# Kernel tuning notes

Measured on AMD Instinct MI355X. Metric: run time of the kernel, lower is better.

Reference implementation:

```python
import jax, jax.numpy as jnp
import numpy as np

# dims: B=batch, N1=in_channels (primary caps), P=pcap_n_dims, N2=n_caps, D=n_dims
B, N1, P, N2, D = 64, 1152, 8, 128, 16
ROUTINGS = 2


def squash(s, axis=-1):
    # squash_factor * unit_vector, with eps-stabilized norm (matches torch.finfo eps)
    sq_norm = jnp.sum(s * s, axis=axis, keepdims=True)
    norm = jnp.sqrt(sq_norm + jnp.finfo(s.dtype).eps)
    return (sq_norm / (1.0 + sq_norm)) * (s / norm)


def setup_inputs() -> dict:
    key = jax.random.key(0)
    k1, k2 = jax.random.split(key)
    x = jax.random.normal(k1, (B, N1, P), dtype=jnp.float32)
    # learned transform W: nn.Parameter(torch.randn(1, N1, N2, D, P)); leading 1 dropped
    W = jax.random.normal(k2, (N1, N2, D, P), dtype=jnp.float32)
    return {"x": x, "W": W}


def reference(x, W):
    b, n1 = x.shape[0], x.shape[1]
    n2 = W.shape[1]
    # caps2_predicted[b,i,n,d] = sum_p W[i,n,d,p] * x[b,i,p]  (the tiled batched matmul)
    pred = jnp.einsum('indp,bip->bind', W, x)  # [B, N1, N2, D]
    raw = jnp.zeros((b, n1, n2), dtype=pred.dtype)  # routing logits
    v = None
    for i in range(ROUTINGS):
        c = jax.nn.softmax(raw, axis=2)                  # softmax over output capsules
        s = jnp.einsum('bin,bind->bnd', c, pred)         # weighted sum over input caps
        v = squash(s, axis=-1)                           # [B, N2, D]
        if i < ROUTINGS - 1:
            # agreement: <prediction, output> over the D dimension
            raw = raw + jnp.einsum('bind,bnd->bin', pred, v)
    return v  # [B, n_caps, n_dims]
```

## Files before the change

kernel.cpp:

```cpp
#include <hip/hip_runtime.h>
#include <math.h>

#define B_   64
#define P_   8
#define N1_  1152
#define N2_  128
#define D_   16

#define NSPLIT 16
#define CHUNK  (N1_ / NSPLIT)
#define NIB    (CHUNK / 4)

typedef __attribute__((ext_vector_type(8)))  short bf16x8;
typedef __attribute__((ext_vector_type(4)))  float f32x4;
typedef __attribute__((ext_vector_type(16))) float f32x16;

__device__ inline void split_frag(float4 a0, float4 a1, bf16x8& hi, bf16x8& lo)
{
    float w[8] = {a0.x, a0.y, a0.z, a0.w, a1.x, a1.y, a1.z, a1.w};
#pragma unroll
    for (int j = 0; j < 8; ++j) {
        unsigned ub = __float_as_uint(w[j]);
        hi[j] = (short)(ub >> 16);
        float hif = __uint_as_float(ub & 0xffff0000u);
        float r = w[j] - hif;
        lo[j] = (short)(__float_as_uint(r) >> 16);
    }
}

__device__ inline void split_arr(const float* w, bf16x8& hi, bf16x8& lo)
{
#pragma unroll
    for (int j = 0; j < 8; ++j) {
        unsigned ub = __float_as_uint(w[j]);
        hi[j] = (short)(ub >> 16);
        float hif = __uint_as_float(ub & 0xffff0000u);
        float r = w[j] - hif;
        lo[j] = (short)(__float_as_uint(r) >> 16);
    }
}

__device__ inline void split4_pack(float4 s, uint2& hp, uint2& lp)
{
    float w[4] = {s.x, s.y, s.z, s.w};
    unsigned hs[4], ls[4];
#pragma unroll
    for (int j = 0; j < 4; ++j) {
        unsigned ub = __float_as_uint(w[j]);
        hs[j] = ub >> 16;
        float hif = __uint_as_float(ub & 0xffff0000u);
        float r = w[j] - hif;
        ls[j] = __float_as_uint(r) >> 16;
    }
    hp.x = hs[0] | (hs[1] << 16); hp.y = hs[2] | (hs[3] << 16);
    lp.x = ls[0] | (ls[1] << 16); lp.y = ls[2] | (ls[3] << 16);
}

__device__ inline unsigned short bf16_rne(float x, float& deq)
{
    unsigned ub = __float_as_uint(x);
    unsigned r  = ub + 0x7fffu + ((ub >> 16) & 1u);
    unsigned short us = (unsigned short)(r >> 16);
    deq = __uint_as_float(((unsigned)us) << 16);
    return us;
}

__global__ __launch_bounds__(128) void k0_xt(const float* __restrict__ x,
                                             float* __restrict__ xt,
                                             unsigned short* __restrict__ xth,
                                             unsigned short* __restrict__ xtl,
                                             float* __restrict__ denom)
{
    const int i  = blockIdx.x;
    const int t  = threadIdx.x;
    const int b  = t >> 1, ph = t & 1;
    float4 v = *(const float4*)(x + ((size_t)b * N1_ + i) * P_ + ph * 4);
    const size_t off = (size_t)i * (64 * P_) + b * P_ + ph * 4;
    *(float4*)(xt + off) = v;
    uint2 hp, lp;
    split4_pack(v, hp, lp);
    *(uint2*)(xth + off) = hp;
    *(uint2*)(xtl + off) = lp;
    int z = i * 128 + t;
    if (z < N1_ * 64) denom[z] = 0.f;
}

__global__ __launch_bounds__(256) void k1_s0_mfma(const unsigned short* __restrict__ xth,
                                                  const unsigned short* __restrict__ xtl,
                                                  const float* __restrict__ W,
                                                  float* __restrict__ s0p)
{
    const int tid   = threadIdx.x;
    const int lane  = tid & 63;
    const int wv    = tid >> 6;
    const int col   = lane & 15;
    const int quad  = lane >> 4;
    const int n     = blockIdx.x * 4 + wv;
    const int isp   = blockIdx.y;
    const int ibase = isp * CHUNK;

    f32x4 acc[4];
#pragma unroll
    for (int bt = 0; bt < 4; ++bt) acc[bt] = (f32x4){0.f, 0.f, 0.f, 0.f};

    for (int ib = 0; ib < NIB; ++ib) {
        const int iq = ibase + ib * 4 + quad;
        const float* wp = W + ((size_t)iq * N2_ + n) * (D_ * P_) + col * P_;
        float4 wa = *(const float4*)wp;
        float4 wb = *(const float4*)(wp + 4);
        bf16x8 ahi, alo;
        split_frag(wa, wb, ahi, alo);
#pragma unroll
        for (int bt = 0; bt < 4; ++bt) {
            const int b = bt * 16 + col;
            const size_t xo = (size_t)iq * (64 * P_) + b * P_;
            bf16x8 bhi = *(const bf16x8*)(xth + xo);
            bf16x8 blo = *(const bf16x8*)(xtl + xo);
            acc[bt] = __builtin_amdgcn_mfma_f32_16x16x32_bf16(ahi, bhi, acc[bt], 0, 0, 0);
            acc[bt] = __builtin_amdgcn_mfma_f32_16x16x32_bf16(ahi, blo, acc[bt], 0, 0, 0);
            acc[bt] = __builtin_amdgcn_mfma_f32_16x16x32_bf16(alo, bhi, acc[bt], 0, 0, 0);
        }
    }
#pragma unroll
    for (int bt = 0; bt < 4; ++bt) {
        const int b = bt * 16 + col;
        float4 v = make_float4(acc[bt][0], acc[bt][1], acc[bt][2], acc[bt][3]);
        *(float4*)(s0p + (size_t)isp * (B_ * N2_ * D_) + (size_t)b * (N2_ * D_)
                   + n * D_ + quad * 4) = v;
    }
}

__global__ __launch_bounds__(256) void k2_squash(const float* __restrict__ spart,
                                                 float* __restrict__ vout,
                                                 unsigned short* __restrict__ v0h,
                                                 unsigned short* __restrict__ v0l,
                                                 float scale, int nsplit)
{
    int idx = blockIdx.x * 256 + threadIdx.x;
    float4 s = make_float4(0.f, 0.f, 0.f, 0.f);
    for (int sp = 0; sp < nsplit; ++sp) {
        float4 t = *(const float4*)(spart + (size_t)sp * (B_ * N2_ * D_) + (size_t)idx * 4);
        s.x += t.x; s.y += t.y; s.z += t.z; s.w += t.w;
    }
    s.x *= scale; s.y *= scale; s.z *= scale; s.w *= scale;
    float sq = s.x * s.x + s.y * s.y + s.z * s.z + s.w * s.w;
    sq += __shfl_xor(sq, 1);
    sq += __shfl_xor(sq, 2);
    float norm = sqrtf(sq + 1.1920929e-7f);
    float f = (sq / (1.f + sq)) / norm;
    float4 o = make_float4(s.x * f, s.y * f, s.z * f, s.w * f);
    *(float4*)(vout + (size_t)idx * 4) = o;
    if (v0h) {
        uint2 hp, lp;
        split4_pack(o, hp, lp);
        *(uint2*)(v0h + (size_t)idx * 4) = hp;
        *(uint2*)(v0l + (size_t)idx * 4) = lp;
    }
}

__global__ __launch_bounds__(256) void k3a2_mfma32(const float* __restrict__ xt,
                                                   const float* __restrict__ W,
                                                   const unsigned short* __restrict__ v0h,
                                                   const unsigned short* __restrict__ v0l,
                                                   unsigned short* __restrict__ e_t,
                                                   float* __restrict__ denom)
{
    const int tid  = threadIdx.x;
    const int lane = tid & 63;
    const int wv   = tid >> 6;
    const int m    = lane & 31;
    const int kh   = lane >> 5;
    const int isub = m >> 3;
    const int p    = m & 7;
    const int i0   = blockIdx.y * 4;
    const int nbase = blockIdx.x * 32 + wv * 8;

    float4 xq0[4], xq1[4];
#pragma unroll
    for (int is = 0; is < 4; ++is) {
        const float* xp = xt + (size_t)(i0 + is) * (64 * P_) + m * 8 + kh * 4;
        xq0[is] = *(const float4*)xp;
        xq1[is] = *(const float4*)(xp + 256);
    }

    float dacc[4] = {0.f, 0.f, 0.f, 0.f};

#pragma unroll 1
    for (int nt = 0; nt < 8; ++nt) {
        const int n = nbase + nt;

        bf16x8 vhi[2], vlo[2];
#pragma unroll
        for (int bt = 0; bt < 2; ++bt) {
            const size_t vo = (size_t)(bt * 32 + m) * (N2_ * D_) + n * D_ + kh * 8;
            vhi[bt] = *(const bf16x8*)(v0h + vo);
            vlo[bt] = *(const bf16x8*)(v0l + vo);
        }

        const float* wp = W + ((size_t)(i0 + isub) * N2_ + n) * (D_ * P_) + kh * 64 + p;
        float a[8];
#pragma unroll
        for (int j = 0; j < 8; ++j) a[j] = wp[8 * j];
        bf16x8 ahi, alo;
        split_arr(a, ahi, alo);

        f32x16 acc0, acc1;
#pragma unroll
        for (int r = 0; r < 16; ++r) { acc0[r] = 0.f; acc1[r] = 0.f; }
        acc0 = __builtin_amdgcn_mfma_f32_32x32x16_bf16(ahi, vhi[0], acc0, 0, 0, 0);
        acc0 = __builtin_amdgcn_mfma_f32_32x32x16_bf16(ahi, vlo[0], acc0, 0, 0, 0);
        acc0 = __builtin_amdgcn_mfma_f32_32x32x16_bf16(alo, vhi[0], acc0, 0, 0, 0);
        acc1 = __builtin_amdgcn_mfma_f32_32x32x16_bf16(ahi, vhi[1], acc1, 0, 0, 0);
        acc1 = __builtin_amdgcn_mfma_f32_32x32x16_bf16(ahi, vlo[1], acc1, 0, 0, 0);
        acc1 = __builtin_amdgcn_mfma_f32_32x32x16_bf16(alo, vhi[1], acc1, 0, 0, 0);

#pragma unroll
        for (int is = 0; is < 4; ++is) {
            float r0 = acc0[4 * is] * xq0[is].x + acc0[4 * is + 1] * xq0[is].y
                     + acc0[4 * is + 2] * xq0[is].z + acc0[4 * is + 3] * xq0[is].w;
            float r1 = acc1[4 * is] * xq1[is].x + acc1[4 * is + 1] * xq1[is].y
                     + acc1[4 * is + 2] * xq1[is].z + acc1[4 * is + 3] * xq1[is].w;
            r0 += __shfl_xor(r0, 32);
            r1 += __shfl_xor(r1, 32);
            float e = __expf(kh ? r1 : r0);
            float er;
            unsigned short eb = bf16_rne(e, er);
            e_t[(size_t)(i0 + is) * (N2_ * 64) + n * 64 + kh * 32 + m] = eb;
            dacc[is] += er;
        }
    }

    __shared__ float dred[4][4][64];
#pragma unroll
    for (int is = 0; is < 4; ++is) dred[wv][is][kh * 32 + m] = dacc[is];
    __syncthreads();
    {
        const int is = tid >> 6;
        const int b  = tid & 63;
        float s = dred[0][is][b] + dred[1][is][b] + dred[2][is][b] + dred[3][is][b];
        atomicAdd(&denom[(size_t)(i0 + is) * 64 + b], s);
    }
}

__global__ __launch_bounds__(256) void k3c_s1_mfma(const float* __restrict__ xt,
                                                   const float* __restrict__ W,
                                                   const unsigned short* __restrict__ e_t,
                                                   const float* __restrict__ denom,
                                                   float* __restrict__ s1p)
{
    const int tid   = threadIdx.x;
    const int lane  = tid & 63;
    const int wv    = tid >> 6;
    const int col   = lane & 15;
    const int quad  = lane >> 4;
    const int n     = blockIdx.x * 4 + wv;
    const int isp   = blockIdx.y;
    const int ibase = isp * CHUNK;

    f32x4 acc[4];
#pragma unroll
    for (int bt = 0; bt < 4; ++bt) acc[bt] = (f32x4){0.f, 0.f, 0.f, 0.f};

    for (int ib = 0; ib < NIB; ++ib) {
        const int iq = ibase + ib * 4 + quad;
        const float* wp = W + ((size_t)iq * N2_ + n) * (D_ * P_) + col * P_;
        float4 wa = *(const float4*)wp;
        float4 wb = *(const float4*)(wp + 4);
        bf16x8 ahi, alo;
        split_frag(wa, wb, ahi, alo);
#pragma unroll
        for (int bt = 0; bt < 4; ++bt) {
            const int b = bt * 16 + col;
            const float* xp = xt + (size_t)iq * (64 * P_) + b * P_;
            float4 xa = *(const float4*)xp;
            float4 xb = *(const float4*)(xp + 4);
            float e  = __uint_as_float((unsigned)e_t[((size_t)iq * N2_ + n) * 64 + b] << 16);
            float dv = denom[(size_t)iq * 64 + b];
            float c  = e * __builtin_amdgcn_rcpf(dv);
            float4 ya = make_float4(xa.x * c, xa.y * c, xa.z * c, xa.w * c);
            float4 yb = make_float4(xb.x * c, xb.y * c, xb.z * c, xb.w * c);
            bf16x8 bhi, blo;
            split_frag(ya, yb, bhi, blo);
            acc[bt] = __builtin_amdgcn_mfma_f32_16x16x32_bf16(ahi, bhi, acc[bt], 0, 0, 0);
            acc[bt] = __builtin_amdgcn_mfma_f32_16x16x32_bf16(ahi, blo, acc[bt], 0, 0, 0);
            acc[bt] = __builtin_amdgcn_mfma_f32_16x16x32_bf16(alo, bhi, acc[bt], 0, 0, 0);
        }
    }
#pragma unroll
    for (int bt = 0; bt < 4; ++bt) {
        const int b = bt * 16 + col;
        float4 v = make_float4(acc[bt][0], acc[bt][1], acc[bt][2], acc[bt][3]);
        *(float4*)(s1p + (size_t)isp * (B_ * N2_ * D_) + (size_t)b * (N2_ * D_)
                   + n * D_ + quad * 4) = v;
    }
}

extern "C" void kernel_launch(void* const* d_in, const int* in_sizes, int n_in,
                              void* d_out, int out_size, void* d_ws, size_t ws_size,
                              hipStream_t stream)
{
    const float* x = (const float*)d_in[0];
    const float* W = (const float*)d_in[1];
    float* out = (float*)d_out;

    float* s_part = (float*)d_ws;
    float* v0     = s_part + (size_t)NSPLIT * B_ * N2_ * D_;
    float* xt     = v0 + B_ * N2_ * D_;
    float* denom  = xt + (size_t)N1_ * 64 * P_;
    unsigned short* xth = (unsigned short*)(denom + (size_t)N1_ * 64);
    unsigned short* xtl = xth + (size_t)N1_ * 64 * P_;
    unsigned short* v0h = xtl + (size_t)N1_ * 64 * P_;
    unsigned short* v0l = v0h + (size_t)B_ * N2_ * D_;
    unsigned short* e_t = v0l + (size_t)B_ * N2_ * D_;

    k0_xt       <<<N1_,               128, 0, stream>>>(x, xt, xth, xtl, denom);
    k1_s0_mfma  <<<dim3(32, NSPLIT),  256, 0, stream>>>(xth, xtl, W, s_part);
    k2_squash   <<<128,               256, 0, stream>>>(s_part, v0, v0h, v0l, 1.f / 128.f, NSPLIT);
    k3a2_mfma32 <<<dim3(4, N1_ / 4),  256, 0, stream>>>(xt, W, v0h, v0l, e_t, denom);
    k3c_s1_mfma <<<dim3(32, NSPLIT),  256, 0, stream>>>(xt, W, e_t, denom, s_part);
    k2_squash   <<<128,               256, 0, stream>>>(s_part, out, nullptr, nullptr, 1.f, NSPLIT);
}
```

Before: 188.4 us.

## Drop x transpose kernel; read x directly and give k3a2 full-n blocks

Removes the k0 transpose/split kernel and has the MFMA kernels read x in its original layout, splitting it to bf16 hi/lo in registers instead. k3a2 now uses 1024-thread blocks covering all 128 output capsules for a 4-row slab of i. The per-block denominator sum is written directly instead of through atomics, which also removes the need to zero denom beforehand. This saves one launch and the workspace traffic for xt, xth and xtl. In exchange, x reads are strided by N1*P across the batch, and k1 redoes the split arithmetic in each block.

```diff
diff --git a/kernel.cpp b/kernel.cpp
--- a/kernel.cpp
+++ b/kernel.cpp
@@ -65,28 +65,7 @@
     return us;
 }
 
-__global__ __launch_bounds__(128) void k0_xt(const float* __restrict__ x,
-                                             float* __restrict__ xt,
-                                             unsigned short* __restrict__ xth,
-                                             unsigned short* __restrict__ xtl,
-                                             float* __restrict__ denom)
-{
-    const int i  = blockIdx.x;
-    const int t  = threadIdx.x;
-    const int b  = t >> 1, ph = t & 1;
-    float4 v = *(const float4*)(x + ((size_t)b * N1_ + i) * P_ + ph * 4);
-    const size_t off = (size_t)i * (64 * P_) + b * P_ + ph * 4;
-    *(float4*)(xt + off) = v;
-    uint2 hp, lp;
-    split4_pack(v, hp, lp);
-    *(uint2*)(xth + off) = hp;
-    *(uint2*)(xtl + off) = lp;
-    int z = i * 128 + t;
-    if (z < N1_ * 64) denom[z] = 0.f;
-}
-
-__global__ __launch_bounds__(256) void k1_s0_mfma(const unsigned short* __restrict__ xth,
-                                                  const unsigned short* __restrict__ xtl,
+__global__ __launch_bounds__(256) void k1_s0_mfma(const float* __restrict__ x,
                                                   const float* __restrict__ W,
                                                   float* __restrict__ s0p)
 {
@@ -113,9 +92,11 @@
 #pragma unroll
         for (int bt = 0; bt < 4; ++bt) {
             const int b = bt * 16 + col;
-            const size_t xo = (size_t)iq * (64 * P_) + b * P_;
-            bf16x8 bhi = *(const bf16x8*)(xth + xo);
-            bf16x8 blo = *(const bf16x8*)(xtl + xo);
+            const float* xp = x + ((size_t)b * N1_ + iq) * P_;
+            float4 xa = *(const float4*)xp;
+            float4 xb = *(const float4*)(xp + 4);
+            bf16x8 bhi, blo;
+            split_frag(xa, xb, bhi, blo);
             acc[bt] = __builtin_amdgcn_mfma_f32_16x16x32_bf16(ahi, bhi, acc[bt], 0, 0, 0);
             acc[bt] = __builtin_amdgcn_mfma_f32_16x16x32_bf16(ahi, blo, acc[bt], 0, 0, 0);
             acc[bt] = __builtin_amdgcn_mfma_f32_16x16x32_bf16(alo, bhi, acc[bt], 0, 0, 0);
@@ -158,12 +139,12 @@
     }
 }
 
-__global__ __launch_bounds__(256) void k3a2_mfma32(const float* __restrict__ xt,
-                                                   const float* __restrict__ W,
-                                                   const unsigned short* __restrict__ v0h,
-                                                   const unsigned short* __restrict__ v0l,
-                                                   unsigned short* __restrict__ e_t,
-                                                   float* __restrict__ denom)
+__global__ __launch_bounds__(1024) void k3a2_mfma32(const float* __restrict__ x,
+                                                    const float* __restrict__ W,
+                                                    const unsigned short* __restrict__ v0h,
+                                                    const unsigned short* __restrict__ v0l,
+                                                    unsigned short* __restrict__ e_t,
+                                                    float* __restrict__ denom)
 {
     const int tid  = threadIdx.x;
     const int lane = tid & 63;
@@ -172,15 +153,14 @@
     const int kh   = lane >> 5;
     const int isub = m >> 3;
     const int p    = m & 7;
-    const int i0   = blockIdx.y * 4;
-    const int nbase = blockIdx.x * 32 + wv * 8;
+    const int i0   = blockIdx.x * 4;
+    const int nbase = wv * 8;
 
     float4 xq0[4], xq1[4];
 #pragma unroll
     for (int is = 0; is < 4; ++is) {
-        const float* xp = xt + (size_t)(i0 + is) * (64 * P_) + m * 8 + kh * 4;
-        xq0[is] = *(const float4*)xp;
-        xq1[is] = *(const float4*)(xp + 256);
+        xq0[is] = *(const float4*)(x + ((size_t)m * N1_ + i0 + is) * P_ + kh * 4);
+        xq1[is] = *(const float4*)(x + ((size_t)(32 + m) * N1_ + i0 + is) * P_ + kh * 4);
     }
 
     float dacc[4] = {0.f, 0.f, 0.f, 0.f};
@@ -230,19 +210,21 @@
         }
     }
 
-    __shared__ float dred[4][4][64];
+    __shared__ float dred[16][4][64];
 #pragma unroll
     for (int is = 0; is < 4; ++is) dred[wv][is][kh * 32 + m] = dacc[is];
     __syncthreads();
-    {
+    if (tid < 256) {
         const int is = tid >> 6;
         const int b  = tid & 63;
-        float s = dred[0][is][b] + dred[1][is][b] + dred[2][is][b] + dred[3][is][b];
-        atomicAdd(&denom[(size_t)(i0 + is) * 64 + b], s);
-    }
-}
-
-__global__ __launch_bounds__(256) void k3c_s1_mfma(const float* __restrict__ xt,
+        float s = 0.f;
+#pragma unroll
+        for (int w = 0; w < 16; ++w) s += dred[w][is][b];
+        denom[(size_t)(i0 + is) * 64 + b] = s;
+    }
+}
+
+__global__ __launch_bounds__(256) void k3c_s1_mfma(const float* __restrict__ x,
                                                    const float* __restrict__ W,
                                                    const unsigned short* __restrict__ e_t,
                                                    const float* __restrict__ denom,
@@ -271,7 +253,7 @@
 #pragma unroll
         for (int bt = 0; bt < 4; ++bt) {
             const int b = bt * 16 + col;
-            const float* xp = xt + (size_t)iq * (64 * P_) + b * P_;
+            const float* xp = x + ((size_t)b * N1_ + iq) * P_;
             float4 xa = *(const float4*)xp;
             float4 xb = *(const float4*)(xp + 4);
             float e  = __uint_as_float((unsigned)e_t[((size_t)iq * N2_ + n) * 64 + b] << 16);
@@ -305,18 +287,14 @@
 
     float* s_part = (float*)d_ws;
     float* v0     = s_part + (size_t)NSPLIT * B_ * N2_ * D_;
-    float* xt     = v0 + B_ * N2_ * D_;
-    float* denom  = xt + (size_t)N1_ * 64 * P_;
-    unsigned short* xth = (unsigned short*)(denom + (size_t)N1_ * 64);
-    unsigned short* xtl = xth + (size_t)N1_ * 64 * P_;
-    unsigned short* v0h = xtl + (size_t)N1_ * 64 * P_;
+    float* denom  = v0 + B_ * N2_ * D_;
+    unsigned short* v0h = (unsigned short*)(denom + (size_t)N1_ * 64);
     unsigned short* v0l = v0h + (size_t)B_ * N2_ * D_;
     unsigned short* e_t = v0l + (size_t)B_ * N2_ * D_;
 
-    k0_xt       <<<N1_,               128, 0, stream>>>(x, xt, xth, xtl, denom);
-    k1_s0_mfma  <<<dim3(32, NSPLIT),  256, 0, stream>>>(xth, xtl, W, s_part);
+    k1_s0_mfma  <<<dim3(32, NSPLIT),  256, 0, stream>>>(x, W, s_part);
     k2_squash   <<<128,               256, 0, stream>>>(s_part, v0, v0h, v0l, 1.f / 128.f, NSPLIT);
-    k3a2_mfma32 <<<dim3(4, N1_ / 4),  256, 0, stream>>>(xt, W, v0h, v0l, e_t, denom);
-    k3c_s1_mfma <<<dim3(32, NSPLIT),  256, 0, stream>>>(xt, W, e_t, denom, s_part);
+    k3a2_mfma32 <<<N1_ / 4,          1024, 0, stream>>>(x, W, v0h, v0l, e_t, denom);
+    k3c_s1_mfma <<<dim3(32, NSPLIT),  256, 0, stream>>>(x, W, e_t, denom, s_part);
     k2_squash   <<<128,               256, 0, stream>>>(s_part, out, nullptr, nullptr, 1.f, NSPLIT);
 }
```

After: 232.2 us. 1.23x slower.
